# Kernel optimization log

Measured on AMD Instinct MI355X. Metric: run time of the kernel, lower is better.

The kernel has to match this reference:

```python
import jax, jax.numpy as jnp
import numpy as np

B, T, E, H, N_TAGS = 128, 512, 256, 512, 32
START, END = 30, 31


def setup_inputs() -> dict:
    key = jax.random.key(0)
    ks = jax.random.split(key, 12)
    s = 1.0 / np.sqrt(H)

    def w(k, shape):
        return jax.random.normal(k, shape, jnp.float32) * s

    X = jax.random.normal(ks[0], (B, T, E), jnp.float32)
    length = jnp.sort(jax.random.randint(ks[1], (B,), T // 2, T + 1))[::-1]
    masks = (jnp.arange(T)[None, :] < length[:, None]).astype(jnp.float32)
    W_ih_f, W_hh_f, b_f = w(ks[2], (4 * H, E)), w(ks[3], (4 * H, H)), w(ks[4], (4 * H,))
    W_ih_b, W_hh_b, b_b = w(ks[5], (4 * H, E)), w(ks[6], (4 * H, H)), w(ks[7], (4 * H,))
    W_out, b_out = w(ks[8], (N_TAGS, 2 * H)), w(ks[9], (N_TAGS,))
    transitions = jax.random.normal(ks[10], (N_TAGS, N_TAGS), jnp.float32)
    transitions = transitions.at[:, START].set(-1e4).at[END, :].set(-1e4)
    return dict(X=X, masks=masks, length=length,
                W_ih_f=W_ih_f, W_hh_f=W_hh_f, b_f=b_f,
                W_ih_b=W_ih_b, W_hh_b=W_hh_b, b_b=b_b,
                W_out=W_out, b_out=b_out, transitions=transitions)


def _lstm_dir(Xt, mt, Wih, Whh, b, reverse):
    # Xt: [T,B,E], mt: [T,B,1]. Masked update emulates pack_padded_sequence
    # (state frozen on pad; for reverse dir, state stays zero until last valid token).
    h0 = jnp.zeros((Xt.shape[1], H), Xt.dtype)

    def step(carry, inp):
        h, c = carry
        x, m = inp
        gates = x @ Wih.T + h @ Whh.T + b  # [B,4H], torch gate order i,f,g,o
        i, f, g, o = jnp.split(gates, 4, axis=-1)
        i, f, o = jax.nn.sigmoid(i), jax.nn.sigmoid(f), jax.nn.sigmoid(o)
        g = jnp.tanh(g)
        c_new = f * c + i * g
        h_new = o * jnp.tanh(c_new)
        h = m * h_new + (1.0 - m) * h
        c = m * c_new + (1.0 - m) * c
        return (h, c), h

    _, hs = jax.lax.scan(step, (h0, h0), (Xt, mt), reverse=reverse)
    return hs  # [T,B,H]


def reference(X, masks, length, W_ih_f, W_hh_f, b_f, W_ih_b, W_hh_b, b_b, W_out, b_out, transitions):
    Xt = X.transpose(1, 0, 2)            # [T,B,E]
    mT = masks.T                          # [T,B]
    mt = mT[:, :, None]
    hf = _lstm_dir(Xt, mt, W_ih_f, W_hh_f, b_f, False)
    hb = _lstm_dir(Xt, mt, W_ih_b, W_hh_b, b_b, True)
    emis = jnp.concatenate([hf, hb], axis=-1) @ W_out.T + b_out  # [T,B,n_tags]

    # Viterbi forward recurrence with masking
    alphas0 = emis[0] + transitions[START]  # [B,n]

    def vstep(alphas, inp):
        e, m = inp  # e: [B,n], m: [B,1]
        scores = alphas[:, :, None] + transitions[None] + e[:, None, :]  # [B,from,to]
        alphas = m * scores.max(axis=1) + (1.0 - m) * alphas
        return alphas, jnp.argmax(scores, axis=1)

    alphas, bps = jax.lax.scan(vstep, alphas0, (emis[1:], mt[1:]))
    final = alphas + transitions[:, END]
    max_end_scores = final.max(axis=1)      # [B]
    end_tags = jnp.argmax(final, axis=1)    # [B]

    # Masked backtrace: bps[k] is the backpointer into position k+1
    def bstep(cur, inp):
        bp, m = inp  # bp: [B,n], m: [B]
        prev = jnp.where(m > 0, jnp.take_along_axis(bp, cur[:, None], axis=1)[:, 0], cur)
        return prev, prev

    _, outs = jax.lax.scan(bstep, end_tags, (bps, mT[1:]), reverse=True)  # outs[k]=tag at pos k
    tags = jnp.concatenate([outs, end_tags[None]], axis=0).T              # [B,T]
    tags = jnp.where(masks > 0, tags, -1)
    return max_end_scores, tags
```

## Files before the change

### kernel.cpp

```cpp
#include <hip/hip_runtime.h>
#include <cfloat>
#include <cmath>

#define Bn 128
#define Tn 512
#define En 256
#define Hn 512
#define NTAGS 32
#define CHK 64
#define NCHK 12

#define OFF_HF 0
#define OFF_HB 131072
#define OFF_CF 262144
#define OFF_CB 327680
#define OFF_EF 393216
#define OFF_EB 2490368

__device__ __forceinline__ void gll16(const float* g, float* l) {
  __builtin_amdgcn_global_load_lds(
      (const __attribute__((address_space(1))) void*)g,
      (__attribute__((address_space(3))) void*)l, 16, 0, 0);
}

__global__ __launch_bounds__(512, 2) void lstm_step_k(
    const float* __restrict__ X, const float* __restrict__ masks,
    const float* __restrict__ Wih_f, const float* __restrict__ Whh_f, const float* __restrict__ bias_f,
    const float* __restrict__ Wih_b, const float* __restrict__ Whh_b, const float* __restrict__ bias_b,
    const float* __restrict__ Wout, float* __restrict__ ws, int s)
{
  __shared__ __align__(16) float WT[768 * 16];
  __shared__ __align__(16) float HX[2][CHK * Bn];
  __shared__ __align__(16) float GL[Bn * 17];
  __shared__ __align__(16) float WoL[512];
  __shared__ __align__(16) float RS[16 * 32];

  const int tid   = threadIdx.x;
  const int blk   = blockIdx.x;
  const int lane  = tid & 63;
  const int wid   = __builtin_amdgcn_readfirstlane(tid >> 6);
  const int cg    = wid & 1;
  const int kt    = wid >> 1;
  const int bg    = lane & 31;
  const int khalf = lane >> 5;

  const int dir = blk >> 7;
  const int bbk = blk & 127;
  const int t = dir ? (Tn - 1 - s) : s;
  const float* Wih  = dir ? Wih_b  : Wih_f;
  const float* Whh  = dir ? Whh_b  : Whh_f;
  const float* bias = dir ? bias_b : bias_f;
  float* hbuf = ws + (dir ? OFF_HB : OFF_HF);
  float* cbuf = ws + (dir ? OFF_CB : OFF_CF);
  const int rbuf = (s + 1) & 1;
  const int wbuf = s & 1;
  const float* hprev = hbuf + rbuf * (Hn * Bn);
  float*       hnext = hbuf + wbuf * (Hn * Bn);
  const int hidx0 = bbk * 4;

  const int etag = bbk & 31;
  const int ebq  = bbk >> 5;

  #pragma unroll
  for (int r = 0; r < 4; ++r) {
    const int item = r * 512 + tid;
    gll16(hprev + item * 4, &HX[0][item * 4]);
  }
  {
    const int lc = tid & 15;
    const int kw = tid >> 4;
    const int row = (lc >> 2) * Hn + hidx0 + (lc & 3);
    #pragma unroll
    for (int i = 0; i < 6; ++i) {
      const int k = (kw + i * 32) * 4;
      float4 w4;
      if (k < Hn) w4 = *(const float4*)&Whh[(size_t)row * Hn + k];
      else        w4 = *(const float4*)&Wih[(size_t)row * En + (k - Hn)];
      WT[(k + 0) * 16 + lc] = w4.x; WT[(k + 1) * 16 + lc] = w4.y;
      WT[(k + 2) * 16 + lc] = w4.z; WT[(k + 3) * 16 + lc] = w4.w;
    }
  }
  if (tid < 128) {
    const float4 wo = *(const float4*)&Wout[(size_t)etag * (2 * Hn) + dir * Hn + tid * 4];
    *(float4*)&WoL[tid * 4] = wo;
  }
  __syncthreads();

  float acc[4][8];
  #pragma unroll
  for (int m = 0; m < 4; ++m)
    #pragma unroll
    for (int n = 0; n < 8; ++n) acc[m][n] = 0.f;
  float eacc = 0.f;

  const int xbq = tid & 127;
  const int xeg = tid >> 7;

  #pragma unroll 1
  for (int c = 0; c < NCHK; ++c) {
    const int nxt = c + 1;
    float4 st[4];
    if (nxt < 8) {
      const float* src = hprev + nxt * (CHK * Bn);
      float* dst = &HX[nxt & 1][0];
      #pragma unroll
      for (int r = 0; r < 4; ++r) {
        const int item = r * 512 + tid;
        gll16(src + item * 4, dst + item * 4);
      }
    } else if (nxt < NCHK) {
      const int e0 = (nxt - 8) * CHK;
      #pragma unroll
      for (int r = 0; r < 4; ++r)
        st[r] = *(const float4*)&X[(size_t)xbq * (Tn * En) + (size_t)t * En + e0 + xeg * 16 + r * 4];
    }

    {
      const float* HXc = &HX[c & 1][0];
      #pragma unroll
      for (int j = 0; j < 8; ++j) {
        const int l = kt * 16 + j * 2 + khalf;
        const float4 av = *(const float4*)&HXc[l * Bn + bg * 4];
        const float4 wa = *(const float4*)&WT[(c * 64 + l) * 16 + cg * 8];
        const float4 wb = *(const float4*)&WT[(c * 64 + l) * 16 + cg * 8 + 4];
        const float avf[4] = {av.x, av.y, av.z, av.w};
        const float wvf[8] = {wa.x, wa.y, wa.z, wa.w, wb.x, wb.y, wb.z, wb.w};
        #pragma unroll
        for (int m = 0; m < 4; ++m)
          #pragma unroll
          for (int n = 0; n < 8; ++n)
            acc[m][n] += avf[m] * wvf[n];
      }
      if (c < 8) {
        const int be = tid & 31;
        const int kq = tid >> 5;
        #pragma unroll
        for (int j = 0; j < 4; ++j)
          eacc += HXc[(kq * 4 + j) * Bn + ebq * 32 + be] * WoL[c * 64 + kq * 4 + j];
      }
    }

    if (nxt >= 8 && nxt < NCHK) {
      float* dst = &HX[nxt & 1][0];
      #pragma unroll
      for (int r = 0; r < 4; ++r) {
        const int el = xeg * 16 + r * 4;
        dst[(el + 0) * Bn + xbq] = st[r].x;
        dst[(el + 1) * Bn + xbq] = st[r].y;
        dst[(el + 2) * Bn + xbq] = st[r].z;
        dst[(el + 3) * Bn + xbq] = st[r].w;
      }
    }
    __syncthreads();
  }

  float* P = &HX[0][0];
  const int ks = kt * 2 + khalf;
  #pragma unroll
  for (int n = 0; n < 8; ++n)
    *(float4*)&P[ks * 2048 + (cg * 8 + n) * 128 + bg * 4] =
        make_float4(acc[0][n], acc[1][n], acc[2][n], acc[3][n]);
  RS[(tid >> 5) * 32 + (tid & 31)] = eacc;
  __syncthreads();
  {
    const int b  = tid & 127;
    const int cq = tid >> 7;
    float g4[4] = {0.f, 0.f, 0.f, 0.f};
    #pragma unroll
    for (int k2 = 0; k2 < 8; ++k2)
      #pragma unroll
      for (int ci = 0; ci < 4; ++ci)
        g4[ci] += P[k2 * 2048 + (cq * 4 + ci) * 128 + b];
    #pragma unroll
    for (int ci = 0; ci < 4; ++ci)
      GL[b * 17 + cq * 4 + ci] = g4[ci];
  }
  __syncthreads();

  {
    const int b  = tid & 127;
    const int hh = tid >> 7;
    const int hidx = hidx0 + hh;
    const float gi = GL[b * 17 + hh]      + bias[hidx];
    const float gf = GL[b * 17 + 4 + hh]  + bias[Hn + hidx];
    const float gc = GL[b * 17 + 8 + hh]  + bias[2 * Hn + hidx];
    const float go = GL[b * 17 + 12 + hh] + bias[3 * Hn + hidx];
    const float iv = 1.f / (1.f + expf(-gi));
    const float fv = 1.f / (1.f + expf(-gf));
    const float gv = tanhf(gc);
    const float ov = 1.f / (1.f + expf(-go));
    const float cold = cbuf[hidx * Bn + b];
    const float cnew = fv * cold + iv * gv;
    const float hold = hprev[hidx * Bn + b];
    const float hnew = ov * tanhf(cnew);
    const float m = masks[(size_t)b * Tn + t];
    hnext[hidx * Bn + b] = (m > 0.f) ? hnew : hold;
    cbuf[hidx * Bn + b]  = (m > 0.f) ? cnew : cold;
  }

  if (tid < 32 && s > 0) {
    const int tprev = dir ? (Tn - s) : (s - 1);
    float* Edst = ws + (dir ? OFF_EB : OFF_EF);
    float v = 0.f;
    #pragma unroll
    for (int g = 0; g < 16; ++g) v += RS[g * 32 + tid];
    Edst[(size_t)tprev * (NTAGS * Bn) + etag * Bn + ebq * 32 + tid] = v;
  }
}

__global__ __launch_bounds__(512) void emis_final_k(const float* __restrict__ Wout,
                                                    float* __restrict__ ws)
{
  __shared__ float RSf[16 * Bn];
  const int tid = threadIdx.x;
  const int dir = blockIdx.x >> 5;
  const int tag = blockIdx.x & 31;
  const float* hsrc = ws + (dir ? OFF_HB : OFF_HF) + 1 * (Hn * Bn);
  const int tprev = dir ? 0 : (Tn - 1);
  const float* wrow = Wout + (size_t)tag * (2 * Hn) + dir * Hn;
  float* Edst = ws + (dir ? OFF_EB : OFF_EF);
  const int bq = tid & 31;
  const int kg = tid >> 5;
  float4 a4 = make_float4(0.f, 0.f, 0.f, 0.f);
  #pragma unroll 4
  for (int kk = 0; kk < 32; ++kk) {
    const int k = kg * 32 + kk;
    const float w = wrow[k];
    const float4 h4 = *(const float4*)&hsrc[k * Bn + bq * 4];
    a4.x += h4.x * w; a4.y += h4.y * w; a4.z += h4.z * w; a4.w += h4.w * w;
  }
  *(float4*)&RSf[kg * Bn + bq * 4] = a4;
  __syncthreads();
  if (tid < 128) {
    float v = 0.f;
    #pragma unroll
    for (int g = 0; g < 16; ++g) v += RSf[g * Bn + tid];
    Edst[(size_t)tprev * (NTAGS * Bn) + tag * Bn + tid] = v;
  }
}

__global__ __launch_bounds__(64) void viterbi_k(
    const float* __restrict__ Ef, const float* __restrict__ Eb,
    const float* __restrict__ bout, const float* __restrict__ trans,
    const float* __restrict__ masks, float* __restrict__ out)
{
  const int b = blockIdx.x;
  const int l = threadIdx.x;
  __shared__ float tr[32][32];
  __shared__ float al[32];
  __shared__ float msk[512];
  __shared__ unsigned char bp[512][32];
  __shared__ int tseq[512];

  for (int i = l; i < 1024; i += 64) tr[i >> 5][i & 31] = trans[i];
  for (int i = l; i < 512; i += 64) msk[i] = masks[(size_t)b * 512 + i];
  __syncthreads();

  const int j  = l & 31;
  const int hi = l >> 5;
  if (l < 32)
    al[j] = Ef[(size_t)j * Bn + b] + Eb[(size_t)j * Bn + b] + bout[j] + tr[30][j];
  __syncthreads();

  for (int t = 1; t < 512; ++t) {
    float pmax = -FLT_MAX; int pidx = 0;
    #pragma unroll
    for (int ii = 0; ii < 16; ++ii) {
      const int i = hi * 16 + ii;
      const float sc = al[i] + tr[i][j];
      if (sc > pmax) { pmax = sc; pidx = i; }
    }
    const float omax = __shfl_down(pmax, 32);
    const int   oidx = __shfl_down(pidx, 32);
    if (l < 32) {
      if (omax > pmax) { pmax = omax; pidx = oidx; }
      bp[t][j] = (unsigned char)pidx;
      const float e = Ef[(size_t)t * (NTAGS * Bn) + j * Bn + b]
                    + Eb[(size_t)t * (NTAGS * Bn) + j * Bn + b] + bout[j];
      const float na = pmax + e;
      if (msk[t] > 0.f) al[j] = na;
    }
    __syncthreads();
  }

  float fv; int fidx;
  if (l < 32) { fv = al[l] + tr[l][31]; fidx = l; }
  else        { fv = -FLT_MAX; fidx = 1 << 30; }
  #pragma unroll
  for (int off = 16; off >= 1; off >>= 1) {
    const float v2 = __shfl_xor(fv, off);
    const int   i2 = __shfl_xor(fidx, off);
    if (v2 > fv || (v2 == fv && i2 < fidx)) { fv = v2; fidx = i2; }
  }
  if (l == 0) {
    out[b] = fv;
    int cur = fidx;
    tseq[511] = cur;
    for (int t = 511; t >= 1; --t) {
      const int prev = (msk[t] > 0.f) ? (int)bp[t][cur] : cur;
      tseq[t - 1] = prev;
      cur = prev;
    }
  }
  __syncthreads();
  for (int t = l; t < 512; t += 64) {
    const float tv = (msk[t] > 0.f) ? (float)tseq[t] : -1.0f;
    out[Bn + (size_t)b * 512 + t] = tv;
  }
}

extern "C" void kernel_launch(void* const* d_in, const int* in_sizes, int n_in,
                              void* d_out, int out_size, void* d_ws, size_t ws_size,
                              hipStream_t stream) {
  const float* X      = (const float*)d_in[0];
  const float* masks  = (const float*)d_in[1];
  const float* Wih_f  = (const float*)d_in[3];
  const float* Whh_f  = (const float*)d_in[4];
  const float* bf     = (const float*)d_in[5];
  const float* Wih_b  = (const float*)d_in[6];
  const float* Whh_b  = (const float*)d_in[7];
  const float* bb     = (const float*)d_in[8];
  const float* Wout   = (const float*)d_in[9];
  const float* bout   = (const float*)d_in[10];
  const float* trans  = (const float*)d_in[11];
  float* ws  = (float*)d_ws;
  float* out = (float*)d_out;

  hipMemsetAsync(d_ws, 0, (size_t)OFF_EF * sizeof(float), stream);

  for (int s = 0; s < Tn; ++s)
    lstm_step_k<<<256, 512, 0, stream>>>(X, masks, Wih_f, Whh_f, bf,
                                         Wih_b, Whh_b, bb, Wout, ws, s);
  emis_final_k<<<64, 512, 0, stream>>>(Wout, ws);
  viterbi_k<<<128, 64, 0, stream>>>(ws + OFF_EF, ws + OFF_EB, bout, trans, masks, out);
}
```

Before: 11.28 ms.

## Triple-buffer LSTM step loads with manual waitcnt and widen per-thread tile

Reworks the per-timestep LSTM kernel's K loop into a three-stage LDS ring with prefetch distance two. It uses explicit vmcnt/lgkmcnt waits and raw barriers in place of __syncthreads. Each wave now computes all 16 gate columns over a narrower K slice, with a shuffle-based reduction across half-waves, and the emission dot product is folded into the main FMA loop. Mask, bias and old state loads are hoisted to the kernel start to hide their latency. The risks are higher register pressure from the 64-accumulator tile, and fragile hand-placed wait counts that could race if the load counts are off.

```diff
diff --git a/kernel.cpp b/kernel.cpp
--- a/kernel.cpp
+++ b/kernel.cpp
@@ -7,8 +7,6 @@
 #define En 256
 #define Hn 512
 #define NTAGS 32
-#define CHK 64
-#define NCHK 12
 
 #define OFF_HF 0
 #define OFF_HB 131072
@@ -21,6 +19,24 @@
   __builtin_amdgcn_global_load_lds(
       (const __attribute__((address_space(1))) void*)g,
       (__attribute__((address_space(3))) void*)l, 16, 0, 0);
+}
+
+__device__ __forceinline__ void wait_vm4() {
+  asm volatile("s_waitcnt vmcnt(4)" ::: "memory");
+  __builtin_amdgcn_sched_barrier(0);
+}
+__device__ __forceinline__ void wait_vm0() {
+  asm volatile("s_waitcnt vmcnt(0)" ::: "memory");
+  __builtin_amdgcn_sched_barrier(0);
+}
+__device__ __forceinline__ void wait_lgkm0() {
+  asm volatile("s_waitcnt lgkmcnt(0)" ::: "memory");
+  __builtin_amdgcn_sched_barrier(0);
+}
+__device__ __forceinline__ void barrier_raw() {
+  __builtin_amdgcn_sched_barrier(0);
+  __builtin_amdgcn_s_barrier();
+  __builtin_amdgcn_sched_barrier(0);
 }
 
 __global__ __launch_bounds__(512, 2) void lstm_step_k(
@@ -30,19 +46,18 @@
     const float* __restrict__ Wout, float* __restrict__ ws, int s)
 {
   __shared__ __align__(16) float WT[768 * 16];
-  __shared__ __align__(16) float HX[2][CHK * Bn];
-  __shared__ __align__(16) float GL[Bn * 17];
+  __shared__ __align__(16) float HXf[3 * 64 * 128];
+  __shared__ __align__(16) float GL[128 * 17];
   __shared__ __align__(16) float WoL[512];
-  __shared__ __align__(16) float RS[16 * 32];
-
-  const int tid   = threadIdx.x;
-  const int blk   = blockIdx.x;
-  const int lane  = tid & 63;
-  const int wid   = __builtin_amdgcn_readfirstlane(tid >> 6);
-  const int cg    = wid & 1;
-  const int kt    = wid >> 1;
-  const int bg    = lane & 31;
-  const int khalf = lane >> 5;
+  __shared__ __align__(16) float RS[8 * 128];
+
+  const int tid  = threadIdx.x;
+  const int blk  = blockIdx.x;
+  const int lane = tid & 63;
+  const int wid  = __builtin_amdgcn_readfirstlane(tid >> 6);
+  const int kq   = wid;
+  const int bg   = lane & 31;
+  const int kh   = lane >> 5;
 
   const int dir = blk >> 7;
   const int bbk = blk & 127;
@@ -57,14 +72,36 @@
   const float* hprev = hbuf + rbuf * (Hn * Bn);
   float*       hnext = hbuf + wbuf * (Hn * Bn);
   const int hidx0 = bbk * 4;
-
   const int etag = bbk & 31;
   const int ebq  = bbk >> 5;
 
+  const int pb  = tid & 127;
+  const int phh = tid >> 7;
+  const int hidxp = hidx0 + phh;
+  const float mval = masks[(size_t)pb * Tn + t];
+  const float bi  = bias[hidxp];
+  const float bf_ = bias[Hn + hidxp];
+  const float bg_ = bias[2 * Hn + hidxp];
+  const float bo_ = bias[3 * Hn + hidxp];
+  const float cold = cbuf[hidxp * Bn + pb];
+  const float hold = hprev[hidxp * Bn + pb];
+  float wol_v = 0.f;
+  if (tid < 128) {
+    const float4 wo = *(const float4*)&Wout[(size_t)etag * (2 * Hn) + dir * Hn + tid * 4];
+    *(float4*)&WoL[tid * 4] = wo;
+    wol_v = wo.x;
+  }
+  (void)wol_v;
+
   #pragma unroll
   for (int r = 0; r < 4; ++r) {
     const int item = r * 512 + tid;
-    gll16(hprev + item * 4, &HX[0][item * 4]);
+    gll16(hprev + item * 4, &HXf[0 * 8192 + item * 4]);
+  }
+  #pragma unroll
+  for (int r = 0; r < 4; ++r) {
+    const int item = r * 512 + tid;
+    gll16(hprev + 8192 + item * 4, &HXf[1 * 8192 + item * 4]);
   }
   {
     const int lc = tid & 15;
@@ -80,87 +117,116 @@
       WT[(k + 2) * 16 + lc] = w4.z; WT[(k + 3) * 16 + lc] = w4.w;
     }
   }
-  if (tid < 128) {
-    const float4 wo = *(const float4*)&Wout[(size_t)etag * (2 * Hn) + dir * Hn + tid * 4];
-    *(float4*)&WoL[tid * 4] = wo;
-  }
-  __syncthreads();
-
-  float acc[4][8];
+  asm volatile("s_waitcnt vmcnt(4) lgkmcnt(0)" ::: "memory");
+  __builtin_amdgcn_sched_barrier(0);
+  barrier_raw();
+
+  float acc[4][16];
   #pragma unroll
   for (int m = 0; m < 4; ++m)
     #pragma unroll
-    for (int n = 0; n < 8; ++n) acc[m][n] = 0.f;
-  float eacc = 0.f;
+    for (int n = 0; n < 16; ++n) acc[m][n] = 0.f;
+  float eac[4] = {0.f, 0.f, 0.f, 0.f};
 
   const int xbq = tid & 127;
   const int xeg = tid >> 7;
+  float4 xA[4], xB[4];
+
+#define STORE_X(REGS, CW)                                              \
+  {                                                                    \
+    float* dst_ = &HXf[((CW) % 3) * 8192];                             \
+    _Pragma("unroll")                                                  \
+    for (int r = 0; r < 4; ++r) {                                      \
+      const int el = xeg * 16 + r * 4;                                 \
+      dst_[(el + 0) * 128 + xbq] = REGS[r].x;                          \
+      dst_[(el + 1) * 128 + xbq] = REGS[r].y;                          \
+      dst_[(el + 2) * 128 + xbq] = REGS[r].z;                          \
+      dst_[(el + 3) * 128 + xbq] = REGS[r].w;                          \
+    }                                                                  \
+  }
 
   #pragma unroll 1
-  for (int c = 0; c < NCHK; ++c) {
-    const int nxt = c + 1;
-    float4 st[4];
-    if (nxt < 8) {
-      const float* src = hprev + nxt * (CHK * Bn);
-      float* dst = &HX[nxt & 1][0];
+  for (int c = 0; c < 12; ++c) {
+    if (c + 2 <= 7) {
+      const float* src = hprev + (c + 2) * 8192;
+      float* dst = &HXf[((c + 2) % 3) * 8192];
       #pragma unroll
       for (int r = 0; r < 4; ++r) {
         const int item = r * 512 + tid;
         gll16(src + item * 4, dst + item * 4);
       }
-    } else if (nxt < NCHK) {
-      const int e0 = (nxt - 8) * CHK;
+    } else if (c + 2 <= 11) {
+      const int e0 = (c + 2 - 8) * 64;
+      const float* xsrc = &X[(size_t)xbq * (Tn * En) + (size_t)t * En + e0 + xeg * 16];
+      if (((c + 2) & 1) == 0) {
+        #pragma unroll
+        for (int r = 0; r < 4; ++r) xA[r] = *(const float4*)(xsrc + r * 4);
+      } else {
+        #pragma unroll
+        for (int r = 0; r < 4; ++r) xB[r] = *(const float4*)(xsrc + r * 4);
+      }
+    }
+
+    {
+      const float* HXc = &HXf[(c % 3) * 8192];
+      const int kw0 = c * 64;
       #pragma unroll
-      for (int r = 0; r < 4; ++r)
-        st[r] = *(const float4*)&X[(size_t)xbq * (Tn * En) + (size_t)t * En + e0 + xeg * 16 + r * 4];
-    }
-
-    {
-      const float* HXc = &HX[c & 1][0];
-      #pragma unroll
-      for (int j = 0; j < 8; ++j) {
-        const int l = kt * 16 + j * 2 + khalf;
-        const float4 av = *(const float4*)&HXc[l * Bn + bg * 4];
-        const float4 wa = *(const float4*)&WT[(c * 64 + l) * 16 + cg * 8];
-        const float4 wb = *(const float4*)&WT[(c * 64 + l) * 16 + cg * 8 + 4];
-        const float avf[4] = {av.x, av.y, av.z, av.w};
-        const float wvf[8] = {wa.x, wa.y, wa.z, wa.w, wb.x, wb.y, wb.z, wb.w};
+      for (int j = 0; j < 4; ++j) {
+        const int kl = kq * 8 + j * 2 + kh;
+        const float4 av = *(const float4*)&HXc[kl * 128 + bg * 4];
+        const float4 w0 = *(const float4*)&WT[(kw0 + kl) * 16];
+        const float4 w1 = *(const float4*)&WT[(kw0 + kl) * 16 + 4];
+        const float4 w2 = *(const float4*)&WT[(kw0 + kl) * 16 + 8];
+        const float4 w3 = *(const float4*)&WT[(kw0 + kl) * 16 + 12];
+        const float a_[4]  = {av.x, av.y, av.z, av.w};
+        const float w_[16] = {w0.x, w0.y, w0.z, w0.w, w1.x, w1.y, w1.z, w1.w,
+                              w2.x, w2.y, w2.z, w2.w, w3.x, w3.y, w3.z, w3.w};
         #pragma unroll
         for (int m = 0; m < 4; ++m)
           #pragma unroll
-          for (int n = 0; n < 8; ++n)
-            acc[m][n] += avf[m] * wvf[n];
+          for (int n = 0; n < 16; ++n)
+            acc[m][n] += a_[m] * w_[n];
+        if (c < 8) {
+          const float wo = WoL[kw0 + kl];
+          eac[0] += a_[0] * wo; eac[1] += a_[1] * wo;
+          eac[2] += a_[2] * wo; eac[3] += a_[3] * wo;
+        }
       }
-      if (c < 8) {
-        const int be = tid & 31;
-        const int kq = tid >> 5;
-        #pragma unroll
-        for (int j = 0; j < 4; ++j)
-          eacc += HXc[(kq * 4 + j) * Bn + ebq * 32 + be] * WoL[c * 64 + kq * 4 + j];
+    }
+
+    if (c < 11) {
+      if (c <= 6) {
+        wait_vm4();
+      } else if (c <= 9) {
+        wait_vm4();
+        if (((c + 1) & 1) == 0) { STORE_X(xA, c + 1) } else { STORE_X(xB, c + 1) }
+        wait_lgkm0();
+      } else {
+        wait_vm0();
+        STORE_X(xB, 11)
+        wait_lgkm0();
       }
-    }
-
-    if (nxt >= 8 && nxt < NCHK) {
-      float* dst = &HX[nxt & 1][0];
-      #pragma unroll
-      for (int r = 0; r < 4; ++r) {
-        const int el = xeg * 16 + r * 4;
-        dst[(el + 0) * Bn + xbq] = st[r].x;
-        dst[(el + 1) * Bn + xbq] = st[r].y;
-        dst[(el + 2) * Bn + xbq] = st[r].z;
-        dst[(el + 3) * Bn + xbq] = st[r].w;
-      }
-    }
-    __syncthreads();
-  }
-
-  float* P = &HX[0][0];
-  const int ks = kt * 2 + khalf;
-  #pragma unroll
-  for (int n = 0; n < 8; ++n)
-    *(float4*)&P[ks * 2048 + (cg * 8 + n) * 128 + bg * 4] =
-        make_float4(acc[0][n], acc[1][n], acc[2][n], acc[3][n]);
-  RS[(tid >> 5) * 32 + (tid & 31)] = eacc;
+      barrier_raw();
+    }
+  }
+#undef STORE_X
+
+  #pragma unroll
+  for (int m = 0; m < 4; ++m)
+    #pragma unroll
+    for (int n = 0; n < 16; ++n)
+      acc[m][n] += __shfl_xor(acc[m][n], 32);
+  #pragma unroll
+  for (int m = 0; m < 4; ++m) eac[m] += __shfl_xor(eac[m], 32);
+
+  float* P = &HXf[0];
+  if (kh == 0) {
+    #pragma unroll
+    for (int n = 0; n < 16; ++n)
+      *(float4*)&P[kq * 2048 + n * 128 + bg * 4] =
+          make_float4(acc[0][n], acc[1][n], acc[2][n], acc[3][n]);
+    *(float4*)&RS[kq * 128 + bg * 4] = make_float4(eac[0], eac[1], eac[2], eac[3]);
+  }
   __syncthreads();
   {
     const int b  = tid & 127;
@@ -178,33 +244,27 @@
   __syncthreads();
 
   {
-    const int b  = tid & 127;
-    const int hh = tid >> 7;
-    const int hidx = hidx0 + hh;
-    const float gi = GL[b * 17 + hh]      + bias[hidx];
-    const float gf = GL[b * 17 + 4 + hh]  + bias[Hn + hidx];
-    const float gc = GL[b * 17 + 8 + hh]  + bias[2 * Hn + hidx];
-    const float go = GL[b * 17 + 12 + hh] + bias[3 * Hn + hidx];
+    const float gi = GL[pb * 17 + phh]       + bi;
+    const float gf = GL[pb * 17 + 4 + phh]   + bf_;
+    const float gc = GL[pb * 17 + 8 + phh]   + bg_;
+    const float go = GL[pb * 17 + 12 + phh]  + bo_;
     const float iv = 1.f / (1.f + expf(-gi));
     const float fv = 1.f / (1.f + expf(-gf));
     const float gv = tanhf(gc);
     const float ov = 1.f / (1.f + expf(-go));
-    const float cold = cbuf[hidx * Bn + b];
     const float cnew = fv * cold + iv * gv;
-    const float hold = hprev[hidx * Bn + b];
     const float hnew = ov * tanhf(cnew);
-    const float m = masks[(size_t)b * Tn + t];
-    hnext[hidx * Bn + b] = (m > 0.f) ? hnew : hold;
-    cbuf[hidx * Bn + b]  = (m > 0.f) ? cnew : cold;
-  }
-
-  if (tid < 32 && s > 0) {
+    hnext[hidxp * Bn + pb] = (mval > 0.f) ? hnew : hold;
+    cbuf[hidxp * Bn + pb]  = (mval > 0.f) ? cnew : cold;
+  }
+
+  if (s > 0 && ebq == 0 && tid < 128) {
     const int tprev = dir ? (Tn - s) : (s - 1);
     float* Edst = ws + (dir ? OFF_EB : OFF_EF);
     float v = 0.f;
     #pragma unroll
-    for (int g = 0; g < 16; ++g) v += RS[g * 32 + tid];
-    Edst[(size_t)tprev * (NTAGS * Bn) + etag * Bn + ebq * 32 + tid] = v;
+    for (int g = 0; g < 8; ++g) v += RS[g * 128 + tid];
+    Edst[(size_t)tprev * (NTAGS * Bn) + etag * Bn + tid] = v;
   }
 }
 
```

Measured after the change: 14.62 ms. +29.6%, slower.

## Read LSTM operands directly from global memory and double block count per step

Applied to the files above, without the earlier changes.

The per-step LSTM kernel stops staging h, X and transposed weights in LDS. Each thread now loads float4 operands straight from global memory, with the k-split reduced by a lane shuffle before a smaller LDS reduction. Each block now owns 2 hidden units instead of 4, so each launch uses 512 blocks. Mask, bias and old state are prefetched up front, and the emission partial sum is computed only by one block quarter. This is meant to remove the LDS staging, the weight transposes and the per-chunk barriers, and to raise occupancy. The cost is more redundant global and L2 traffic for h and X across blocks.

```diff
diff --git a/kernel.cpp b/kernel.cpp
--- a/kernel.cpp
+++ b/kernel.cpp
@@ -7,8 +7,6 @@
 #define En 256
 #define Hn 512
 #define NTAGS 32
-#define CHK 64
-#define NCHK 12
 
 #define OFF_HF 0
 #define OFF_HB 131072
@@ -17,194 +15,176 @@
 #define OFF_EF 393216
 #define OFF_EB 2490368
 
-__device__ __forceinline__ void gll16(const float* g, float* l) {
-  __builtin_amdgcn_global_load_lds(
-      (const __attribute__((address_space(1))) void*)g,
-      (__attribute__((address_space(3))) void*)l, 16, 0, 0);
-}
-
-__global__ __launch_bounds__(512, 2) void lstm_step_k(
+__global__ __launch_bounds__(512, 4) void lstm_step_k(
     const float* __restrict__ X, const float* __restrict__ masks,
     const float* __restrict__ Wih_f, const float* __restrict__ Whh_f, const float* __restrict__ bias_f,
     const float* __restrict__ Wih_b, const float* __restrict__ Whh_b, const float* __restrict__ bias_b,
     const float* __restrict__ Wout, float* __restrict__ ws, int s)
 {
-  __shared__ __align__(16) float WT[768 * 16];
-  __shared__ __align__(16) float HX[2][CHK * Bn];
-  __shared__ __align__(16) float GL[Bn * 17];
-  __shared__ __align__(16) float WoL[512];
-  __shared__ __align__(16) float RS[16 * 32];
-
-  const int tid   = threadIdx.x;
-  const int blk   = blockIdx.x;
-  const int lane  = tid & 63;
-  const int wid   = __builtin_amdgcn_readfirstlane(tid >> 6);
-  const int cg    = wid & 1;
-  const int kt    = wid >> 1;
-  const int bg    = lane & 31;
-  const int khalf = lane >> 5;
-
-  const int dir = blk >> 7;
-  const int bbk = blk & 127;
+  __shared__ __align__(16) float P[8 * 8 * 128];
+  __shared__ __align__(16) float GL[128 * 9];
+  __shared__ __align__(16) float RS[8 * 128];
+
+  const int tid  = threadIdx.x;
+  const int blk  = blockIdx.x;
+  const int lane = tid & 63;
+  const int kq   = __builtin_amdgcn_readfirstlane(tid >> 6);
+  const int bg   = lane & 31;
+  const int kh   = lane >> 5;
+  const int kloc = kq * 8 + kh * 4;
+
+  const int dir = blk >> 8;
+  const int bbk = blk & 255;
   const int t = dir ? (Tn - 1 - s) : s;
   const float* Wih  = dir ? Wih_b  : Wih_f;
   const float* Whh  = dir ? Whh_b  : Whh_f;
   const float* bias = dir ? bias_b : bias_f;
   float* hbuf = ws + (dir ? OFF_HB : OFF_HF);
   float* cbuf = ws + (dir ? OFF_CB : OFF_CF);
-  const int rbuf = (s + 1) & 1;
-  const int wbuf = s & 1;
-  const float* hprev = hbuf + rbuf * (Hn * Bn);
-  float*       hnext = hbuf + wbuf * (Hn * Bn);
-  const int hidx0 = bbk * 4;
-
-  const int etag = bbk & 31;
-  const int ebq  = bbk >> 5;
-
-  #pragma unroll
-  for (int r = 0; r < 4; ++r) {
-    const int item = r * 512 + tid;
-    gll16(hprev + item * 4, &HX[0][item * 4]);
-  }
-  {
-    const int lc = tid & 15;
-    const int kw = tid >> 4;
-    const int row = (lc >> 2) * Hn + hidx0 + (lc & 3);
-    #pragma unroll
-    for (int i = 0; i < 6; ++i) {
-      const int k = (kw + i * 32) * 4;
-      float4 w4;
-      if (k < Hn) w4 = *(const float4*)&Whh[(size_t)row * Hn + k];
-      else        w4 = *(const float4*)&Wih[(size_t)row * En + (k - Hn)];
-      WT[(k + 0) * 16 + lc] = w4.x; WT[(k + 1) * 16 + lc] = w4.y;
-      WT[(k + 2) * 16 + lc] = w4.z; WT[(k + 3) * 16 + lc] = w4.w;
-    }
-  }
-  if (tid < 128) {
-    const float4 wo = *(const float4*)&Wout[(size_t)etag * (2 * Hn) + dir * Hn + tid * 4];
-    *(float4*)&WoL[tid * 4] = wo;
-  }
-  __syncthreads();
+  const float* hprev = hbuf + ((s + 1) & 1) * (Hn * Bn);
+  float*       hnext = hbuf + (s & 1) * (Hn * Bn);
+  const int hidx0 = bbk * 2;
+  const int etag  = bbk & 31;
+  const int ebq   = bbk >> 5;
+
+  const int pb  = tid & 127;
+  const int phh = (tid >> 7) & 1;
+  const int hidxp = hidx0 + phh;
+  float mval = 0.f, bi = 0.f, bf_ = 0.f, bg_ = 0.f, bo_ = 0.f, cold = 0.f, hold = 0.f;
+  if (tid < 256) {
+    mval = masks[(size_t)pb * Tn + t];
+    bi  = bias[hidxp];
+    bf_ = bias[Hn + hidxp];
+    bg_ = bias[2 * Hn + hidxp];
+    bo_ = bias[3 * Hn + hidxp];
+    cold = cbuf[hidxp * Bn + pb];
+    hold = hprev[hidxp * Bn + pb];
+  }
+
+  const float* wor = Wout + (size_t)etag * (2 * Hn) + dir * Hn;
 
   float acc[4][8];
   #pragma unroll
   for (int m = 0; m < 4; ++m)
     #pragma unroll
     for (int n = 0; n < 8; ++n) acc[m][n] = 0.f;
-  float eacc = 0.f;
-
-  const int xbq = tid & 127;
-  const int xeg = tid >> 7;
+  float eac[4] = {0.f, 0.f, 0.f, 0.f};
 
   #pragma unroll 1
-  for (int c = 0; c < NCHK; ++c) {
-    const int nxt = c + 1;
-    float4 st[4];
-    if (nxt < 8) {
-      const float* src = hprev + nxt * (CHK * Bn);
-      float* dst = &HX[nxt & 1][0];
+  for (int c = 0; c < 8; ++c) {
+    const int k0 = c * 64 + kloc;
+    const float* ap = hprev + (size_t)k0 * Bn + bg * 4;
+    const float4 A0 = *(const float4*)(ap);
+    const float4 A1 = *(const float4*)(ap + Bn);
+    const float4 A2 = *(const float4*)(ap + 2 * Bn);
+    const float4 A3 = *(const float4*)(ap + 3 * Bn);
+    float4 Wv[8];
+    #pragma unroll
+    for (int n = 0; n < 8; ++n) {
+      const int cgl = (n >> 1) * Hn + hidx0 + (n & 1);
+      Wv[n] = *(const float4*)(Whh + (size_t)cgl * Hn + k0);
+    }
+    const float4 wo4 = *(const float4*)(wor + k0);
+    const float a0[4] = {A0.x, A0.y, A0.z, A0.w};
+    const float a1[4] = {A1.x, A1.y, A1.z, A1.w};
+    const float a2[4] = {A2.x, A2.y, A2.z, A2.w};
+    const float a3[4] = {A3.x, A3.y, A3.z, A3.w};
+    #pragma unroll
+    for (int n = 0; n < 8; ++n) {
+      const float w0 = Wv[n].x, w1 = Wv[n].y, w2 = Wv[n].z, w3 = Wv[n].w;
       #pragma unroll
-      for (int r = 0; r < 4; ++r) {
-        const int item = r * 512 + tid;
-        gll16(src + item * 4, dst + item * 4);
+      for (int m = 0; m < 4; ++m) {
+        acc[m][n] += a0[m] * w0;
+        acc[m][n] += a1[m] * w1;
+        acc[m][n] += a2[m] * w2;
+        acc[m][n] += a3[m] * w3;
       }
-    } else if (nxt < NCHK) {
-      const int e0 = (nxt - 8) * CHK;
-      #pragma unroll
-      for (int r = 0; r < 4; ++r)
-        st[r] = *(const float4*)&X[(size_t)xbq * (Tn * En) + (size_t)t * En + e0 + xeg * 16 + r * 4];
-    }
-
-    {
-      const float* HXc = &HX[c & 1][0];
-      #pragma unroll
-      for (int j = 0; j < 8; ++j) {
-        const int l = kt * 16 + j * 2 + khalf;
-        const float4 av = *(const float4*)&HXc[l * Bn + bg * 4];
-        const float4 wa = *(const float4*)&WT[(c * 64 + l) * 16 + cg * 8];
-        const float4 wb = *(const float4*)&WT[(c * 64 + l) * 16 + cg * 8 + 4];
-        const float avf[4] = {av.x, av.y, av.z, av.w};
-        const float wvf[8] = {wa.x, wa.y, wa.z, wa.w, wb.x, wb.y, wb.z, wb.w};
-        #pragma unroll
-        for (int m = 0; m < 4; ++m)
-          #pragma unroll
-          for (int n = 0; n < 8; ++n)
-            acc[m][n] += avf[m] * wvf[n];
-      }
-      if (c < 8) {
-        const int be = tid & 31;
-        const int kq = tid >> 5;
-        #pragma unroll
-        for (int j = 0; j < 4; ++j)
-          eacc += HXc[(kq * 4 + j) * Bn + ebq * 32 + be] * WoL[c * 64 + kq * 4 + j];
-      }
-    }
-
-    if (nxt >= 8 && nxt < NCHK) {
-      float* dst = &HX[nxt & 1][0];
-      #pragma unroll
-      for (int r = 0; r < 4; ++r) {
-        const int el = xeg * 16 + r * 4;
-        dst[(el + 0) * Bn + xbq] = st[r].x;
-        dst[(el + 1) * Bn + xbq] = st[r].y;
-        dst[(el + 2) * Bn + xbq] = st[r].z;
-        dst[(el + 3) * Bn + xbq] = st[r].w;
-      }
-    }
-    __syncthreads();
-  }
-
-  float* P = &HX[0][0];
-  const int ks = kt * 2 + khalf;
+    }
+    #pragma unroll
+    for (int m = 0; m < 4; ++m) {
+      eac[m] += a0[m] * wo4.x;
+      eac[m] += a1[m] * wo4.y;
+      eac[m] += a2[m] * wo4.z;
+      eac[m] += a3[m] * wo4.w;
+    }
+  }
+
+  #pragma unroll 1
+  for (int c = 0; c < 4; ++c) {
+    const int e0 = c * 64 + kloc;
+    const float* xp = X + (size_t)(bg * 4) * (Tn * En) + (size_t)t * En + e0;
+    const float4 X0 = *(const float4*)(xp);
+    const float4 X1 = *(const float4*)(xp + Tn * En);
+    const float4 X2 = *(const float4*)(xp + 2 * (Tn * En));
+    const float4 X3 = *(const float4*)(xp + 3 * (Tn * En));
+    float4 Wv[8];
+    #pragma unroll
+    for (int n = 0; n < 8; ++n) {
+      const int cgl = (n >> 1) * Hn + hidx0 + (n & 1);
+      Wv[n] = *(const float4*)(Wih + (size_t)cgl * En + e0);
+    }
+    #pragma unroll
+    for (int n = 0; n < 8; ++n) {
+      const float w0 = Wv[n].x, w1 = Wv[n].y, w2 = Wv[n].z, w3 = Wv[n].w;
+      acc[0][n] += X0.x * w0; acc[0][n] += X0.y * w1; acc[0][n] += X0.z * w2; acc[0][n] += X0.w * w3;
+      acc[1][n] += X1.x * w0; acc[1][n] += X1.y * w1; acc[1][n] += X1.z * w2; acc[1][n] += X1.w * w3;
+      acc[2][n] += X2.x * w0; acc[2][n] += X2.y * w1; acc[2][n] += X2.z * w2; acc[2][n] += X2.w * w3;
+      acc[3][n] += X3.x * w0; acc[3][n] += X3.y * w1; acc[3][n] += X3.z * w2; acc[3][n] += X3.w * w3;
+    }
+  }
+
   #pragma unroll
-  for (int n = 0; n < 8; ++n)
-    *(float4*)&P[ks * 2048 + (cg * 8 + n) * 128 + bg * 4] =
-        make_float4(acc[0][n], acc[1][n], acc[2][n], acc[3][n]);
-  RS[(tid >> 5) * 32 + (tid & 31)] = eacc;
+  for (int m = 0; m < 4; ++m)
+    #pragma unroll
+    for (int n = 0; n < 8; ++n)
+      acc[m][n] += __shfl_xor(acc[m][n], 32);
+  #pragma unroll
+  for (int m = 0; m < 4; ++m) eac[m] += __shfl_xor(eac[m], 32);
+
+  if (kh == 0) {
+    #pragma unroll
+    for (int n = 0; n < 8; ++n)
+      *(float4*)&P[(kq * 8 + n) * 128 + bg * 4] =
+          make_float4(acc[0][n], acc[1][n], acc[2][n], acc[3][n]);
+    *(float4*)&RS[kq * 128 + bg * 4] = make_float4(eac[0], eac[1], eac[2], eac[3]);
+  }
   __syncthreads();
   {
     const int b  = tid & 127;
-    const int cq = tid >> 7;
-    float g4[4] = {0.f, 0.f, 0.f, 0.f};
-    #pragma unroll
-    for (int k2 = 0; k2 < 8; ++k2)
+    const int nq = tid >> 7;
+    #pragma unroll
+    for (int nn = 0; nn < 2; ++nn) {
+      const int n = nq * 2 + nn;
+      float v = 0.f;
       #pragma unroll
-      for (int ci = 0; ci < 4; ++ci)
-        g4[ci] += P[k2 * 2048 + (cq * 4 + ci) * 128 + b];
-    #pragma unroll
-    for (int ci = 0; ci < 4; ++ci)
-      GL[b * 17 + cq * 4 + ci] = g4[ci];
-  }
-  __syncthreads();
-
-  {
-    const int b  = tid & 127;
-    const int hh = tid >> 7;
-    const int hidx = hidx0 + hh;
-    const float gi = GL[b * 17 + hh]      + bias[hidx];
-    const float gf = GL[b * 17 + 4 + hh]  + bias[Hn + hidx];
-    const float gc = GL[b * 17 + 8 + hh]  + bias[2 * Hn + hidx];
-    const float go = GL[b * 17 + 12 + hh] + bias[3 * Hn + hidx];
+      for (int k2 = 0; k2 < 8; ++k2)
+        v += P[(k2 * 8 + n) * 128 + b];
+      GL[b * 9 + n] = v;
+    }
+  }
+  if (s > 0 && ebq == 0 && tid < 128) {
+    const int tprev = dir ? (Tn - s) : (s - 1);
+    float* Edst = ws + (dir ? OFF_EB : OFF_EF);
+    float v = 0.f;
+    #pragma unroll
+    for (int g = 0; g < 8; ++g) v += RS[g * 128 + tid];
+    Edst[(size_t)tprev * (NTAGS * Bn) + etag * Bn + tid] = v;
+  }
+  __syncthreads();
+
+  if (tid < 256) {
+    const float gi = GL[pb * 9 + 0 + phh] + bi;
+    const float gf = GL[pb * 9 + 2 + phh] + bf_;
+    const float gc = GL[pb * 9 + 4 + phh] + bg_;
+    const float go = GL[pb * 9 + 6 + phh] + bo_;
     const float iv = 1.f / (1.f + expf(-gi));
     const float fv = 1.f / (1.f + expf(-gf));
     const float gv = tanhf(gc);
     const float ov = 1.f / (1.f + expf(-go));
-    const float cold = cbuf[hidx * Bn + b];
     const float cnew = fv * cold + iv * gv;
-    const float hold = hprev[hidx * Bn + b];
     const float hnew = ov * tanhf(cnew);
-    const float m = masks[(size_t)b * Tn + t];
-    hnext[hidx * Bn + b] = (m > 0.f) ? hnew : hold;
-    cbuf[hidx * Bn + b]  = (m > 0.f) ? cnew : cold;
-  }
-
-  if (tid < 32 && s > 0) {
-    const int tprev = dir ? (Tn - s) : (s - 1);
-    float* Edst = ws + (dir ? OFF_EB : OFF_EF);
-    float v = 0.f;
-    #pragma unroll
-    for (int g = 0; g < 16; ++g) v += RS[g * 32 + tid];
-    Edst[(size_t)tprev * (NTAGS * Bn) + etag * Bn + ebq * 32 + tid] = v;
+    hnext[hidxp * Bn + pb] = (mval > 0.f) ? hnew : hold;
+    cbuf[hidxp * Bn + pb]  = (mval > 0.f) ? cnew : cold;
   }
 }
 
@@ -329,7 +309,7 @@
   hipMemsetAsync(d_ws, 0, (size_t)OFF_EF * sizeof(float), stream);
 
   for (int s = 0; s < Tn; ++s)
-    lstm_step_k<<<256, 512, 0, stream>>>(X, masks, Wih_f, Whh_f, bf,
+    lstm_step_k<<<512, 512, 0, stream>>>(X, masks, Wih_f, Whh_f, bf,
                                          Wih_b, Whh_b, bb, Wout, ws, s);
   emis_final_k<<<64, 512, 0, stream>>>(Wout, ws);
   viterbi_k<<<128, 64, 0, stream>>>(ws + OFF_EF, ws + OFF_EB, bout, trans, masks, out);
```

Result: slower. 14.08 ms (+24.8%).

## Enlarge per-thread register tile to 8x8 and fuse emission dot into GEMM loop

Applied to the files above, without the earlier changes.

Each thread in the per-timestep LSTM kernel now accumulates an 8-batch by 8-gate tile instead of 4x8. The k dimension is split across half-waves and combined with a cross-lane shuffle, so each wave writes one partial. This raises FMAs per LDS load and halves the partial-sum buffer traffic. The emission projection now reuses the already-loaded hidden activations in the same inner loop, and only one block per tag writes the result. The cost is a larger accumulator set that may spill under the 2-blocks-per-CU launch bound, and emission math repeated across blocks.

```diff
diff --git a/kernel.cpp b/kernel.cpp
--- a/kernel.cpp
+++ b/kernel.cpp
@@ -33,16 +33,15 @@
   __shared__ __align__(16) float HX[2][CHK * Bn];
   __shared__ __align__(16) float GL[Bn * 17];
   __shared__ __align__(16) float WoL[512];
-  __shared__ __align__(16) float RS[16 * 32];
-
-  const int tid   = threadIdx.x;
-  const int blk   = blockIdx.x;
-  const int lane  = tid & 63;
-  const int wid   = __builtin_amdgcn_readfirstlane(tid >> 6);
-  const int cg    = wid & 1;
-  const int kt    = wid >> 1;
-  const int bg    = lane & 31;
-  const int khalf = lane >> 5;
+  __shared__ __align__(16) float RS[8 * Bn];
+
+  const int tid  = threadIdx.x;
+  const int blk  = blockIdx.x;
+  const int lane = tid & 63;
+  const int wid  = __builtin_amdgcn_readfirstlane(tid >> 6);
+  const int bq   = tid & 15;
+  const int cg   = (tid >> 4) & 1;
+  const int ks   = tid >> 5;
 
   const int dir = blk >> 7;
   const int bbk = blk & 127;
@@ -86,12 +85,12 @@
   }
   __syncthreads();
 
-  float acc[4][8];
-  #pragma unroll
-  for (int m = 0; m < 4; ++m)
+  float acc[8][8];
+  #pragma unroll
+  for (int m = 0; m < 8; ++m)
     #pragma unroll
     for (int n = 0; n < 8; ++n) acc[m][n] = 0.f;
-  float eacc = 0.f;
+  float eac[8] = {0.f, 0.f, 0.f, 0.f, 0.f, 0.f, 0.f, 0.f};
 
   const int xbq = tid & 127;
   const int xeg = tid >> 7;
@@ -118,25 +117,25 @@
     {
       const float* HXc = &HX[c & 1][0];
       #pragma unroll
-      for (int j = 0; j < 8; ++j) {
-        const int l = kt * 16 + j * 2 + khalf;
-        const float4 av = *(const float4*)&HXc[l * Bn + bg * 4];
-        const float4 wa = *(const float4*)&WT[(c * 64 + l) * 16 + cg * 8];
-        const float4 wb = *(const float4*)&WT[(c * 64 + l) * 16 + cg * 8 + 4];
-        const float avf[4] = {av.x, av.y, av.z, av.w};
-        const float wvf[8] = {wa.x, wa.y, wa.z, wa.w, wb.x, wb.y, wb.z, wb.w};
+      for (int j = 0; j < 4; ++j) {
+        const int kl = ks * 4 + j;
+        const int kg = c * 64 + kl;
+        const float4 a0 = *(const float4*)&HXc[kl * Bn + bq * 4];
+        const float4 a1 = *(const float4*)&HXc[kl * Bn + 64 + bq * 4];
+        const float4 w0 = *(const float4*)&WT[kg * 16 + cg * 8];
+        const float4 w1 = *(const float4*)&WT[kg * 16 + cg * 8 + 4];
+        const float a_[8] = {a0.x, a0.y, a0.z, a0.w, a1.x, a1.y, a1.z, a1.w};
+        const float w_[8] = {w0.x, w0.y, w0.z, w0.w, w1.x, w1.y, w1.z, w1.w};
         #pragma unroll
-        for (int m = 0; m < 4; ++m)
+        for (int m = 0; m < 8; ++m)
           #pragma unroll
           for (int n = 0; n < 8; ++n)
-            acc[m][n] += avf[m] * wvf[n];
-      }
-      if (c < 8) {
-        const int be = tid & 31;
-        const int kq = tid >> 5;
-        #pragma unroll
-        for (int j = 0; j < 4; ++j)
-          eacc += HXc[(kq * 4 + j) * Bn + ebq * 32 + be] * WoL[c * 64 + kq * 4 + j];
+            acc[m][n] += a_[m] * w_[n];
+        if (c < 8) {
+          const float wo = WoL[kg];
+          #pragma unroll
+          for (int m = 0; m < 8; ++m) eac[m] += a_[m] * wo;
+        }
       }
     }
 
@@ -154,26 +153,49 @@
     __syncthreads();
   }
 
+  #pragma unroll
+  for (int m = 0; m < 8; ++m)
+    #pragma unroll
+    for (int n = 0; n < 8; ++n)
+      acc[m][n] += __shfl_xor(acc[m][n], 32);
+  #pragma unroll
+  for (int m = 0; m < 8; ++m) eac[m] += __shfl_xor(eac[m], 32);
+
   float* P = &HX[0][0];
-  const int ks = kt * 2 + khalf;
-  #pragma unroll
-  for (int n = 0; n < 8; ++n)
-    *(float4*)&P[ks * 2048 + (cg * 8 + n) * 128 + bg * 4] =
-        make_float4(acc[0][n], acc[1][n], acc[2][n], acc[3][n]);
-  RS[(tid >> 5) * 32 + (tid & 31)] = eacc;
+  if ((lane >> 5) == 0) {
+    #pragma unroll
+    for (int n = 0; n < 8; ++n) {
+      *(float4*)&P[wid * 2048 + (cg * 8 + n) * Bn + bq * 4] =
+          make_float4(acc[0][n], acc[1][n], acc[2][n], acc[3][n]);
+      *(float4*)&P[wid * 2048 + (cg * 8 + n) * Bn + 64 + bq * 4] =
+          make_float4(acc[4][n], acc[5][n], acc[6][n], acc[7][n]);
+    }
+    if (cg == 0) {
+      *(float4*)&RS[wid * Bn + bq * 4] = make_float4(eac[0], eac[1], eac[2], eac[3]);
+      *(float4*)&RS[wid * Bn + 64 + bq * 4] = make_float4(eac[4], eac[5], eac[6], eac[7]);
+    }
+  }
   __syncthreads();
   {
     const int b  = tid & 127;
     const int cq = tid >> 7;
-    float g4[4] = {0.f, 0.f, 0.f, 0.f};
-    #pragma unroll
-    for (int k2 = 0; k2 < 8; ++k2)
-      #pragma unroll
-      for (int ci = 0; ci < 4; ++ci)
-        g4[ci] += P[k2 * 2048 + (cq * 4 + ci) * 128 + b];
-    #pragma unroll
-    for (int ci = 0; ci < 4; ++ci)
-      GL[b * 17 + cq * 4 + ci] = g4[ci];
+    #pragma unroll
+    for (int nn = 0; nn < 4; ++nn) {
+      const int n = cq * 4 + nn;
+      float v = 0.f;
+      #pragma unroll
+      for (int k2 = 0; k2 < 8; ++k2)
+        v += P[k2 * 2048 + n * Bn + b];
+      GL[b * 17 + n] = v;
+    }
+  }
+  if (s > 0 && ebq == 0 && tid < 128) {
+    const int tprev = dir ? (Tn - s) : (s - 1);
+    float* Edst = ws + (dir ? OFF_EB : OFF_EF);
+    float v = 0.f;
+    #pragma unroll
+    for (int g = 0; g < 8; ++g) v += RS[g * Bn + tid];
+    Edst[(size_t)tprev * (NTAGS * Bn) + etag * Bn + tid] = v;
   }
   __syncthreads();
 
@@ -196,15 +218,6 @@
     const float m = masks[(size_t)b * Tn + t];
     hnext[hidx * Bn + b] = (m > 0.f) ? hnew : hold;
     cbuf[hidx * Bn + b]  = (m > 0.f) ? cnew : cold;
-  }
-
-  if (tid < 32 && s > 0) {
-    const int tprev = dir ? (Tn - s) : (s - 1);
-    float* Edst = ws + (dir ? OFF_EB : OFF_EF);
-    float v = 0.f;
-    #pragma unroll
-    for (int g = 0; g < 16; ++g) v += RS[g * 32 + tid];
-    Edst[(size_t)tprev * (NTAGS * Bn) + etag * Bn + ebq * 32 + tid] = v;
   }
 }
 
```

New measurement: 12.22 ms (median of 3 runs). 1.08x slower.
